# Kernel optimization log

Measured on AMD Instinct MI355X. Metric: run time of the kernel, lower is better.

Reference implementation:

```python
import jax, jax.numpy as jnp
import numpy as np

N, E, D = 20000, 320000, 256
BN_EPS = 1e-5


def _mlp(h, W1, b1, g, be, W2, b2, relu):
    # Linear(d, 2d) -> BatchNorm1d (training-mode batch stats) -> [ReLU] -> Linear(2d, d)
    h = h @ W1 + b1                              # [N, 2d]
    mu = h.mean(axis=0)
    var = h.var(axis=0)                          # biased, matches torch BN training normalization
    h = (h - mu) * jax.lax.rsqrt(var + BN_EPS) * g + be
    if relu:
        h = jax.nn.relu(h)
    return h @ W2 + b2                           # [N, d]


def _gine_conv(x, edge_index, edge_attr, W1, b1, g, be, W2, b2, relu):
    # PyG GINEConv with eps=0: nn((1+eps)*x + sum_j ReLU(x_j + e_ij))
    src, dst = edge_index[0], edge_index[1]
    msg = jax.nn.relu(x[src] + edge_attr)        # [E, d] gather + fuse
    agg = jax.ops.segment_sum(msg, dst, num_segments=x.shape[0])  # scatter-sum
    return _mlp(x + agg, W1, b1, g, be, W2, b2, relu)


def setup_inputs() -> dict:
    key = jax.random.key(0)
    ks = jax.random.split(key, 32)
    inp = {
        'x': jax.random.normal(ks[0], (N, D), dtype=jnp.float32),
        'edge_index': jax.random.randint(ks[1], (2, E), 0, N, dtype=jnp.int64),
        'edge_attr': jax.random.normal(ks[2], (E, D), dtype=jnp.float32),
        'noise': jax.random.normal(ks[3], (N, D), dtype=jnp.float32),
    }
    # 4 GINE convs: base_gcn, base_gcn2 (with ReLU), gcn_mean, gcn_logstddev (no ReLU)
    for i in range(4):
        k = 4 + 6 * i
        s1 = 1.0 / np.sqrt(D)
        s2 = 1.0 / np.sqrt(2 * D)
        inp[f'W1_{i}'] = jax.random.uniform(ks[k], (D, 2 * D), jnp.float32, -s1, s1)
        inp[f'b1_{i}'] = jax.random.uniform(ks[k + 1], (2 * D,), jnp.float32, -s1, s1)
        inp[f'g_{i}'] = jnp.ones((2 * D,), jnp.float32)
        inp[f'be_{i}'] = jnp.zeros((2 * D,), jnp.float32)
        inp[f'W2_{i}'] = jax.random.uniform(ks[k + 2], (2 * D, D), jnp.float32, -s2, s2)
        inp[f'b2_{i}'] = jax.random.uniform(ks[k + 3], (D,), jnp.float32, -s2, s2)
    return inp


def reference(x, edge_index, edge_attr, noise,
              W1_0, b1_0, g_0, be_0, W2_0, b2_0,
              W1_1, b1_1, g_1, be_1, W2_1, b2_1,
              W1_2, b1_2, g_2, be_2, W2_2, b2_2,
              W1_3, b1_3, g_3, be_3, W2_3, b2_3):
    h = _gine_conv(x, edge_index, edge_attr, W1_0, b1_0, g_0, be_0, W2_0, b2_0, True)
    h = _gine_conv(h, edge_index, edge_attr, W1_1, b1_1, g_1, be_1, W2_1, b2_1, True)
    mean = _gine_conv(h, edge_index, edge_attr, W1_2, b1_2, g_2, be_2, W2_2, b2_2, False)
    logstd = _gine_conv(h, edge_index, edge_attr, W1_3, b1_3, g_3, be_3, W2_3, b2_3, False)
    sampled_z = noise * jnp.exp(logstd) + mean   # reparameterization
    kl = 0.5 / sampled_z.shape[0] * (
        (1.0 + 2.0 * logstd - mean ** 2 - jnp.exp(logstd) ** 2).sum(axis=1).mean()
    )
    return sampled_z, mean, logstd, kl
```

## Files before the change

kernel.cpp:

```cpp
#include <hip/hip_runtime.h>

#define NNODES 20000
#define NEDGES 320000
#define DIM 256
#define DIM2 512
#define MPAD 20096
#define BN_EPS 1e-5f
#define NDTOT (NNODES * DIM)

typedef __attribute__((ext_vector_type(8))) short bf16x8;
typedef __attribute__((ext_vector_type(4))) float f32x4;

typedef __attribute__((address_space(1))) const unsigned char gconst_byte;
typedef __attribute__((address_space(3))) unsigned char lds_byte;

__device__ inline ushort f2bf(float f) {
    unsigned u = __float_as_uint(f);
    u += 0x7FFF + ((u >> 16) & 1);
    return (ushort)(u >> 16);
}
__device__ inline float bf2f(ushort u) {
    return __uint_as_float(((unsigned)u) << 16);
}

__global__ void hist_kernel(const int* __restrict__ ei, int* __restrict__ cnt) {
    int e = blockIdx.x * blockDim.x + threadIdx.x;
    if (e < NEDGES) atomicAdd(&cnt[ei[NEDGES + e]], 1);
}

__global__ __launch_bounds__(256) void scan_kernel(const int* __restrict__ cnt,
                                                   int* __restrict__ off,
                                                   int* __restrict__ cur,
                                                   float* __restrict__ klP) {
    int t = threadIdx.x;
    const int CH = (NNODES + 255) / 256;
    int b0 = t * CH, b1 = min(b0 + CH, NNODES);
    int s = 0;
    for (int i = b0; i < b1; ++i) s += cnt[i];
    __shared__ int sums[256];
    sums[t] = s;
    __syncthreads();
    if (t == 0) {
        int acc = 0;
        for (int i = 0; i < 256; ++i) { int tmp = sums[i]; sums[i] = acc; acc += tmp; }
        off[NNODES] = acc;
        klP[0] = 0.f;
    }
    __syncthreads();
    int run = sums[t];
    for (int i = b0; i < b1; ++i) {
        off[i] = run;
        cur[i] = run;
        run += cnt[i];
    }
}

__global__ void scatter_kernel(const int* __restrict__ ei, int* __restrict__ cur,
                               int* __restrict__ perm_e, int* __restrict__ perm_s) {
    int e = blockIdx.x * blockDim.x + threadIdx.x;
    if (e >= NEDGES) return;
    int d = ei[NEDGES + e];
    int pos = atomicAdd(&cur[d], 1);
    perm_e[pos] = e;
    perm_s[pos] = ei[e];
}

template<bool XF32, bool EAPERM, bool WEA>
__global__ __launch_bounds__(256) void agg_kernel(
        const float* __restrict__ Xf, const ushort* __restrict__ Xh,
        const float* __restrict__ EAf, const ushort* __restrict__ EAh,
        ushort* __restrict__ EAout,
        const int* __restrict__ off, const int* __restrict__ perm_e,
        const int* __restrict__ perm_s, ushort* __restrict__ A16) {
    int wid = (blockIdx.x * blockDim.x + threadIdx.x) >> 6;
    if (wid >= NNODES) return;
    int l = threadIdx.x & 63;
    int s0 = off[wid], s1 = off[wid + 1];
    float4 acc;
    if (XF32) {
        acc = *(const float4*)(Xf + (size_t)wid * DIM + l * 4);
    } else {
        ushort4 v = *(const ushort4*)(Xh + (size_t)wid * DIM + l * 4);
        acc = make_float4(bf2f(v.x), bf2f(v.y), bf2f(v.z), bf2f(v.w));
    }
    #pragma unroll 2
    for (int i = s0; i < s1; ++i) {
        int s = perm_s[i];
        float4 xr, er;
        if (XF32) {
            xr = *(const float4*)(Xf + (size_t)s * DIM + l * 4);
        } else {
            ushort4 v = *(const ushort4*)(Xh + (size_t)s * DIM + l * 4);
            xr = make_float4(bf2f(v.x), bf2f(v.y), bf2f(v.z), bf2f(v.w));
        }
        if (EAPERM) {
            ushort4 v = *(const ushort4*)(EAh + (size_t)i * DIM + l * 4);
            er = make_float4(bf2f(v.x), bf2f(v.y), bf2f(v.z), bf2f(v.w));
        } else {
            int e = perm_e[i];
            er = *(const float4*)(EAf + (size_t)e * DIM + l * 4);
        }
        if (WEA) {
            ushort4 o;
            o.x = f2bf(er.x); o.y = f2bf(er.y); o.z = f2bf(er.z); o.w = f2bf(er.w);
            *(ushort4*)(EAout + (size_t)i * DIM + l * 4) = o;
        }
        acc.x += fmaxf(xr.x + er.x, 0.f);
        acc.y += fmaxf(xr.y + er.y, 0.f);
        acc.z += fmaxf(xr.z + er.z, 0.f);
        acc.w += fmaxf(xr.w + er.w, 0.f);
    }
    ushort4 o;
    o.x = f2bf(acc.x); o.y = f2bf(acc.y); o.z = f2bf(acc.z); o.w = f2bf(acc.w);
    *(ushort4*)(A16 + (size_t)wid * DIM + l * 4) = o;
}

struct WPtrs {
    const float* w[8];
    ushort* o[8];
    int K[8];
    int Nc[8];
};
__global__ __launch_bounds__(256) void wconv_kernel(WPtrs p) {
    int w = blockIdx.x >> 9;
    int idx = ((blockIdx.x & 511) << 8) + threadIdx.x;
    int K = p.K[w], Nc = p.Nc[w];
    int oc = idx / K, ok = idx - oc * K;
    p.o[w][idx] = f2bf(p.w[w][(size_t)ok * Nc + oc]);
}

__global__ __launch_bounds__(64) void wfold_kernel(
        const ushort* __restrict__ WT2_2, const ushort* __restrict__ WT2_3,
        const float* __restrict__ stats,
        const float* __restrict__ g2, const float* __restrict__ be2,
        const float* __restrict__ g3, const float* __restrict__ be3,
        const float* __restrict__ b2_2, const float* __restrict__ b2_3,
        ushort* __restrict__ W2f, float* __restrict__ b2f) {
    const int l = blockIdx.x >> 8;
    const int n = blockIdx.x & 255;
    const int lane = threadIdx.x;
    const float invN = 1.0f / (float)NNODES;
    const ushort* WT = l ? WT2_3 : WT2_2;
    const float* gp = l ? g3 : g2;
    const float* bp = l ? be3 : be2;
    float part = 0.f;
    #pragma unroll
    for (int j = 0; j < 8; ++j) {
        int k = j * 64 + lane;
        int c = l * DIM2 + k;
        float mu = stats[c] * invN;
        float var = stats[1024 + c] * invN - mu * mu;
        float sc = gp[k] * rsqrtf(var + BN_EPS);
        float sh = bp[k] - mu * sc;
        float wv = bf2f(WT[(size_t)n * DIM2 + k]);
        W2f[(size_t)l * 131072 + (size_t)n * DIM2 + k] = f2bf(sc * wv);
        part += sh * wv;
    }
    #pragma unroll
    for (int o = 32; o > 0; o >>= 1) part += __shfl_down(part, o);
    if (lane == 0) b2f[l * 256 + n] = (l ? b2_3[n] : b2_2[n]) + part;
}

template<int K, bool OUT_BF16, bool STATS, bool FINAL>
__global__ __launch_bounds__(256) void mfma_gemm(
        const ushort* __restrict__ A16, int lda,
        const ushort* __restrict__ WT,
        const float* __restrict__ bias, const float* __restrict__ bias2,
        float* __restrict__ Cf, ushort* __restrict__ C16, int ldc,
        float* __restrict__ stats, int Nc, int Mlimit,
        const float* __restrict__ meanP, const float* __restrict__ noiseP,
        float* __restrict__ zP, float* __restrict__ klP) {
    __shared__ ushort As[128 * 64];
    __shared__ ushort Bs[128 * 64];
    const int tid = threadIdx.x;
    const int lane = tid & 63;
    const int wv = tid >> 6, wr = wv >> 1, wc = wv & 1;
    const int l15 = lane & 15, lhi = lane >> 4;
    const int r0 = blockIdx.y * 128, c0 = blockIdx.x * 128;

    const int srow = lane >> 3;
    const int scol = ((lane & 7) ^ srow) * 8;
    const int smask = (l15 & 7) << 4;

    f32x4 acc[4][4] = {};

    for (int k0 = 0; k0 < K; k0 += 64) {
        #pragma unroll
        for (int j = 0; j < 4; ++j) {
            const int jp = j * 4 + wv;
            const ushort* ga = A16 + (size_t)(r0 + jp * 8 + srow) * lda + k0 + scol;
            const ushort* gb = WT + (size_t)(c0 + jp * 8 + srow) * K + k0 + scol;
            __builtin_amdgcn_global_load_lds(
                (gconst_byte*)ga, (lds_byte*)((char*)As + jp * 1024), 16, 0, 0);
            __builtin_amdgcn_global_load_lds(
                (gconst_byte*)gb, (lds_byte*)((char*)Bs + jp * 1024), 16, 0, 0);
        }
        __syncthreads();
        #pragma unroll
        for (int kk = 0; kk < 2; ++kk) {
            bf16x8 a[4], b[4];
            #pragma unroll
            for (int m = 0; m < 4; ++m)
                a[m] = *(const bf16x8*)((const char*)As +
                        (wr * 64 + m * 16 + l15) * 128 + ((kk * 64 + lhi * 16) ^ smask));
            #pragma unroll
            for (int n = 0; n < 4; ++n)
                b[n] = *(const bf16x8*)((const char*)Bs +
                        (wc * 64 + n * 16 + l15) * 128 + ((kk * 64 + lhi * 16) ^ smask));
            #pragma unroll
            for (int m = 0; m < 4; ++m)
                #pragma unroll
                for (int n = 0; n < 4; ++n)
                    acc[m][n] = __builtin_amdgcn_mfma_f32_16x16x32_bf16(
                        a[m], b[n], acc[m][n], 0, 0, 0);
        }
        __syncthreads();
    }

    float bv[4];
    #pragma unroll
    for (int n = 0; n < 4; ++n) {
        int gc = c0 + wc * 64 + n * 16 + l15;
        bv[n] = (gc < DIM2) ? bias[gc] : bias2[gc - DIM2];
    }
    float sm[4] = {0.f, 0.f, 0.f, 0.f}, sq[4] = {0.f, 0.f, 0.f, 0.f};
    float kl = 0.f;
    #pragma unroll
    for (int m = 0; m < 4; ++m) {
        #pragma unroll
        for (int q = 0; q < 4; ++q) {
            int gr = r0 + wr * 64 + m * 16 + lhi * 4 + q;
            if (gr >= Mlimit) continue;
            #pragma unroll
            for (int n = 0; n < 4; ++n) {
                int gc = c0 + wc * 64 + n * 16 + l15;
                float v = acc[m][n][q] + bv[n];
                if (OUT_BF16) C16[(size_t)gr * ldc + gc] = f2bf(v);
                else          Cf[(size_t)gr * ldc + gc] = v;
                if (STATS) { sm[n] += v; sq[n] += v * v; }
                if (FINAL) {
                    size_t idx = (size_t)gr * DIM + gc;
                    float mean = meanP[idx];
                    float nz = noiseP[idx];
                    float e = expf(v);
                    zP[idx] = nz * e + mean;
                    kl += 1.f + 2.f * v - mean * mean - e * e;
                }
            }
        }
    }
    if (STATS) {
        #pragma unroll
        for (int n = 0; n < 4; ++n) {
            float sv = sm[n], qv = sq[n];
            sv += __shfl_xor(sv, 16); sv += __shfl_xor(sv, 32);
            qv += __shfl_xor(qv, 16); qv += __shfl_xor(qv, 32);
            if (lane < 16) {
                int gc = c0 + wc * 64 + n * 16 + l15;
                atomicAdd(&stats[gc], sv);
                atomicAdd(&stats[Nc + gc], qv);
            }
        }
    }
    if (FINAL) {
        #pragma unroll
        for (int o = 32; o > 0; o >>= 1) kl += __shfl_down(kl, o);
        if (lane == 0) {
            const float scale = 0.5f / ((float)NNODES * (float)NNODES);
            atomicAdd(klP, kl * scale);
        }
    }
}

template<int NCOLS>
__global__ __launch_bounds__(256) void bn_apply_kernel(
        ushort* __restrict__ H16, const float* __restrict__ stats,
        const float* __restrict__ g0, const float* __restrict__ be0) {
    const float invN = 1.0f / (float)NNODES;
    const int n4 = NNODES * NCOLS / 4;
    for (int i = blockIdx.x * blockDim.x + threadIdx.x; i < n4;
         i += gridDim.x * blockDim.x) {
        int cbase = (i * 4) & (NCOLS - 1);
        ushort4 u = ((const ushort4*)H16)[i];
        float vv[4] = {bf2f(u.x), bf2f(u.y), bf2f(u.z), bf2f(u.w)};
        #pragma unroll
        for (int k = 0; k < 4; ++k) {
            int c = cbase + k;
            float mu = stats[c] * invN;
            float var = stats[NCOLS + c] * invN - mu * mu;
            float x = (vv[k] - mu) * rsqrtf(var + BN_EPS) * g0[c] + be0[c];
            vv[k] = fmaxf(x, 0.f);
        }
        ushort4 o;
        o.x = f2bf(vv[0]); o.y = f2bf(vv[1]); o.z = f2bf(vv[2]); o.w = f2bf(vv[3]);
        ((ushort4*)H16)[i] = o;
    }
}

extern "C" void kernel_launch(void* const* d_in, const int* in_sizes, int n_in,
                              void* d_out, int out_size, void* d_ws, size_t ws_size,
                              hipStream_t stream) {
    const float* x     = (const float*)d_in[0];
    const int*   ei    = (const int*)d_in[1];
    const float* ea    = (const float*)d_in[2];
    const float* noise = (const float*)d_in[3];
    const float *W1[4], *b1[4], *g[4], *be[4], *W2[4], *b2[4];
    for (int i = 0; i < 4; ++i) {
        W1[i] = (const float*)d_in[4 + 6 * i];
        b1[i] = (const float*)d_in[5 + 6 * i];
        g[i]  = (const float*)d_in[6 + 6 * i];
        be[i] = (const float*)d_in[7 + 6 * i];
        W2[i] = (const float*)d_in[8 + 6 * i];
        b2[i] = (const float*)d_in[9 + 6 * i];
    }
    float* out = (float*)d_out;
    float* klP = out + 3 * NDTOT;

    char* p = (char*)d_ws;
    auto carve = [&](size_t bytes) {
        char* r = p;
        p += (bytes + 255) & ~(size_t)255;
        return r;
    };
    ushort* Braw16 = (ushort*)carve((size_t)MPAD * 1024 * 2);
    ushort* H16    = (ushort*)carve((size_t)MPAD * DIM * 2);
    ushort* A16    = (ushort*)carve((size_t)MPAD * DIM * 2);
    ushort* WT16   = (ushort*)carve((size_t)8 * 131072 * 2);
    ushort* W2f    = (ushort*)carve((size_t)2 * 131072 * 2);
    float*  b2f    = (float*)carve(512 * 4);
    float*  stats  = (float*)carve(4096 * 4 + NNODES * 4);
    int*    cnt    = (int*)(stats + 4096);
    int*    off    = (int*)carve((NNODES + 8) * 4);
    int*    cur    = (int*)carve(NNODES * 4);
    int*    perm_e = (int*)carve(NEDGES * 4);
    int*    perm_s = (int*)carve(NEDGES * 4);
    size_t baseBytes = (size_t)(p - (char*)d_ws);
    ushort* ea16 = (ushort*)p;
    const bool useEa16 = (baseBytes + (size_t)NEDGES * DIM * 2) <= ws_size;

    const int edgeGrid = (NEDGES + 255) / 256;
    const int aggGrid = (NNODES * 64) / 256;

    WPtrs wp;
    for (int i = 0; i < 4; ++i) {
        wp.w[i] = W1[i];     wp.o[i] = WT16 + (size_t)i * 131072;
        wp.K[i] = DIM;       wp.Nc[i] = DIM2;
        wp.w[4 + i] = W2[i]; wp.o[4 + i] = WT16 + (size_t)(4 + i) * 131072;
        wp.K[4 + i] = DIM2;  wp.Nc[4 + i] = DIM;
    }
    hipLaunchKernelGGL(wconv_kernel, dim3(8 * 512), dim3(256), 0, stream, wp);

    hipMemsetAsync(stats, 0, 4096 * 4 + NNODES * 4, stream);
    hipLaunchKernelGGL(hist_kernel, dim3(edgeGrid), dim3(256), 0, stream, ei, cnt);
    hipLaunchKernelGGL(scan_kernel, dim3(1), dim3(256), 0, stream, cnt, off, cur, klP);
    hipLaunchKernelGGL(scatter_kernel, dim3(edgeGrid), dim3(256), 0, stream,
                       ei, cur, perm_e, perm_s);

    dim3 blk(256);
    dim3 gemm1Grid(DIM2 / 128, MPAD / 128);
    dim3 gemm1WGrid(1024 / 128, MPAD / 128);
    dim3 gemm2Grid(DIM / 128, MPAD / 128);
    const float* nf = nullptr;
    float* nfm = nullptr;

    if (useEa16)
        hipLaunchKernelGGL((agg_kernel<true, false, true>), dim3(aggGrid), blk, 0, stream,
                           x, (const ushort*)nullptr, ea, (const ushort*)nullptr, ea16,
                           off, perm_e, perm_s, A16);
    else
        hipLaunchKernelGGL((agg_kernel<true, false, false>), dim3(aggGrid), blk, 0, stream,
                           x, (const ushort*)nullptr, ea, (const ushort*)nullptr, (ushort*)nullptr,
                           off, perm_e, perm_s, A16);
    hipLaunchKernelGGL((mfma_gemm<DIM, true, true, false>), gemm1Grid, blk, 0, stream,
                       A16, DIM, WT16, b1[0], b1[0],
                       nfm, Braw16, DIM2, stats, DIM2, NNODES, nf, nf, nfm, nfm);
    hipLaunchKernelGGL((bn_apply_kernel<DIM2>), dim3(2048), blk, 0, stream,
                       Braw16, stats, g[0], be[0]);
    hipLaunchKernelGGL((mfma_gemm<DIM2, true, false, false>), gemm2Grid, blk, 0, stream,
                       Braw16, DIM2, WT16 + 4 * 131072, b2[0], b2[0],
                       nfm, H16, DIM, nfm, DIM, NNODES, nf, nf, nfm, nfm);

    if (useEa16)
        hipLaunchKernelGGL((agg_kernel<false, true, false>), dim3(aggGrid), blk, 0, stream,
                           (const float*)nullptr, H16, (const float*)nullptr, ea16, (ushort*)nullptr,
                           off, perm_e, perm_s, A16);
    else
        hipLaunchKernelGGL((agg_kernel<false, false, false>), dim3(aggGrid), blk, 0, stream,
                           (const float*)nullptr, H16, ea, (const ushort*)nullptr, (ushort*)nullptr,
                           off, perm_e, perm_s, A16);
    hipLaunchKernelGGL((mfma_gemm<DIM, true, true, false>), gemm1Grid, blk, 0, stream,
                       A16, DIM, WT16 + 1 * 131072, b1[1], b1[1],
                       nfm, Braw16, DIM2, stats + 1024, DIM2, NNODES, nf, nf, nfm, nfm);
    hipLaunchKernelGGL((bn_apply_kernel<DIM2>), dim3(2048), blk, 0, stream,
                       Braw16, stats + 1024, g[1], be[1]);
    hipLaunchKernelGGL((mfma_gemm<DIM2, true, false, false>), gemm2Grid, blk, 0, stream,
                       Braw16, DIM2, WT16 + 5 * 131072, b2[1], b2[1],
                       nfm, H16, DIM, nfm, DIM, NNODES, nf, nf, nfm, nfm);

    if (useEa16)
        hipLaunchKernelGGL((agg_kernel<false, true, false>), dim3(aggGrid), blk, 0, stream,
                           (const float*)nullptr, H16, (const float*)nullptr, ea16, (ushort*)nullptr,
                           off, perm_e, perm_s, A16);
    else
        hipLaunchKernelGGL((agg_kernel<false, false, false>), dim3(aggGrid), blk, 0, stream,
                           (const float*)nullptr, H16, ea, (const ushort*)nullptr, (ushort*)nullptr,
                           off, perm_e, perm_s, A16);
    hipLaunchKernelGGL((mfma_gemm<DIM, true, true, false>), gemm1WGrid, blk, 0, stream,
                       A16, DIM, WT16 + 2 * 131072, b1[2], b1[3],
                       nfm, Braw16, 1024, stats + 2048, 1024, NNODES, nf, nf, nfm, nfm);
    hipLaunchKernelGGL(wfold_kernel, dim3(512), dim3(64), 0, stream,
                       WT16 + 6 * 131072, WT16 + 7 * 131072, stats + 2048,
                       g[2], be[2], g[3], be[3], b2[2], b2[3], W2f, b2f);
    hipLaunchKernelGGL((mfma_gemm<DIM2, false, false, false>), gemm2Grid, blk, 0, stream,
                       Braw16, 1024, W2f, b2f, b2f,
                       out + NDTOT, (ushort*)nullptr, DIM, nfm, DIM, NNODES, nf, nf, nfm, nfm);
    hipLaunchKernelGGL((mfma_gemm<DIM2, false, false, true>), gemm2Grid, blk, 0, stream,
                       Braw16 + 512, 1024, W2f + 131072, b2f + 256, b2f + 256,
                       out + 2 * NDTOT, (ushort*)nullptr, DIM, nfm, DIM, NNODES,
                       out + NDTOT, noise, out, klP);
}
```

Measured before the change: 517.1 us.

## Prefetch edge rows in aggregation, tile weight transpose, narrow GEMM2 column tiles

The aggregation loop now software-pipelines its loads, fetching the next edge's source row and edge attribute while it accumulates the current one. The weight conversion kernel now transposes through a padded 64x64 shared-memory tile, so both global reads and writes are coalesced instead of strided. The GEMM kernel gains a BCOLS template parameter, and the second GEMM of each MLP uses 64-column tiles, doubling its block count over 256 CUs. Narrower tiles give more parallelism but less B reuse per block.

```diff
diff --git a/kernel.cpp b/kernel.cpp
--- a/kernel.cpp
+++ b/kernel.cpp
@@ -76,30 +76,31 @@
     if (wid >= NNODES) return;
     int l = threadIdx.x & 63;
     int s0 = off[wid], s1 = off[wid + 1];
-    float4 acc;
-    if (XF32) {
-        acc = *(const float4*)(Xf + (size_t)wid * DIM + l * 4);
-    } else {
-        ushort4 v = *(const ushort4*)(Xh + (size_t)wid * DIM + l * 4);
-        acc = make_float4(bf2f(v.x), bf2f(v.y), bf2f(v.z), bf2f(v.w));
-    }
-    #pragma unroll 2
-    for (int i = s0; i < s1; ++i) {
-        int s = perm_s[i];
-        float4 xr, er;
-        if (XF32) {
-            xr = *(const float4*)(Xf + (size_t)s * DIM + l * 4);
-        } else {
-            ushort4 v = *(const ushort4*)(Xh + (size_t)s * DIM + l * 4);
-            xr = make_float4(bf2f(v.x), bf2f(v.y), bf2f(v.z), bf2f(v.w));
-        }
+
+    auto loadX = [&](int s) -> float4 {
+        if (XF32) return *(const float4*)(Xf + (size_t)s * DIM + l * 4);
+        ushort4 v = *(const ushort4*)(Xh + (size_t)s * DIM + l * 4);
+        return make_float4(bf2f(v.x), bf2f(v.y), bf2f(v.z), bf2f(v.w));
+    };
+    auto loadE = [&](int i) -> float4 {
         if (EAPERM) {
             ushort4 v = *(const ushort4*)(EAh + (size_t)i * DIM + l * 4);
-            er = make_float4(bf2f(v.x), bf2f(v.y), bf2f(v.z), bf2f(v.w));
-        } else {
-            int e = perm_e[i];
-            er = *(const float4*)(EAf + (size_t)e * DIM + l * 4);
-        }
+            return make_float4(bf2f(v.x), bf2f(v.y), bf2f(v.z), bf2f(v.w));
+        }
+        int e = perm_e[i];
+        return *(const float4*)(EAf + (size_t)e * DIM + l * 4);
+    };
+
+    float4 acc = loadX(wid);
+    if (!XF32) {  }
+
+    int i = s0;
+    float4 xc, ec;
+    if (i < s1) { xc = loadX(perm_s[i]); ec = loadE(i); }
+    while (i < s1) {
+        float4 xr = xc, er = ec;
+        int inext = i + 1;
+        if (inext < s1) { xc = loadX(perm_s[inext]); ec = loadE(inext); }
         if (WEA) {
             ushort4 o;
             o.x = f2bf(er.x); o.y = f2bf(er.y); o.z = f2bf(er.z); o.w = f2bf(er.w);
@@ -109,6 +110,7 @@
         acc.y += fmaxf(xr.y + er.y, 0.f);
         acc.z += fmaxf(xr.z + er.z, 0.f);
         acc.w += fmaxf(xr.w + er.w, 0.f);
+        i = inext;
     }
     ushort4 o;
     o.x = f2bf(acc.x); o.y = f2bf(acc.y); o.z = f2bf(acc.z); o.w = f2bf(acc.w);
@@ -122,11 +124,27 @@
     int Nc[8];
 };
 __global__ __launch_bounds__(256) void wconv_kernel(WPtrs p) {
-    int w = blockIdx.x >> 9;
-    int idx = ((blockIdx.x & 511) << 8) + threadIdx.x;
+    __shared__ float T[64][65];
+    int w = blockIdx.x >> 5;
+    int tile = blockIdx.x & 31;
     int K = p.K[w], Nc = p.Nc[w];
-    int oc = idx / K, ok = idx - oc * K;
-    p.o[w][idx] = f2bf(p.w[w][(size_t)ok * Nc + oc]);
+    int tilesPerRow = Nc >> 6;
+    int tk = (tile / tilesPerRow) << 6;
+    int tc = (tile % tilesPerRow) << 6;
+    int tx = threadIdx.x & 63, ty = threadIdx.x >> 6;
+    const float* in = p.w[w];
+    #pragma unroll
+    for (int r = 0; r < 16; ++r) {
+        int kk = ty + r * 4;
+        T[kk][tx] = in[(size_t)(tk + kk) * Nc + tc + tx];
+    }
+    __syncthreads();
+    ushort* outp = p.o[w];
+    #pragma unroll
+    for (int r = 0; r < 16; ++r) {
+        int cc = ty + r * 4;
+        outp[(size_t)(tc + cc) * K + tk + tx] = f2bf(T[tx][cc]);
+    }
 }
 
 __global__ __launch_bounds__(64) void wfold_kernel(
@@ -161,7 +179,7 @@
     if (lane == 0) b2f[l * 256 + n] = (l ? b2_3[n] : b2_2[n]) + part;
 }
 
-template<int K, bool OUT_BF16, bool STATS, bool FINAL>
+template<int K, int BCOLS, bool OUT_BF16, bool STATS, bool FINAL>
 __global__ __launch_bounds__(256) void mfma_gemm(
         const ushort* __restrict__ A16, int lda,
         const ushort* __restrict__ WT,
@@ -170,60 +188,67 @@
         float* __restrict__ stats, int Nc, int Mlimit,
         const float* __restrict__ meanP, const float* __restrict__ noiseP,
         float* __restrict__ zP, float* __restrict__ klP) {
+    constexpr int NREP = BCOLS / 32;
     __shared__ ushort As[128 * 64];
-    __shared__ ushort Bs[128 * 64];
+    __shared__ ushort Bs[BCOLS * 64];
     const int tid = threadIdx.x;
     const int lane = tid & 63;
     const int wv = tid >> 6, wr = wv >> 1, wc = wv & 1;
     const int l15 = lane & 15, lhi = lane >> 4;
-    const int r0 = blockIdx.y * 128, c0 = blockIdx.x * 128;
+    const int r0 = blockIdx.y * 128, c0 = blockIdx.x * BCOLS;
 
     const int srow = lane >> 3;
     const int scol = ((lane & 7) ^ srow) * 8;
     const int smask = (l15 & 7) << 4;
 
-    f32x4 acc[4][4] = {};
+    f32x4 acc[4][NREP] = {};
 
     for (int k0 = 0; k0 < K; k0 += 64) {
         #pragma unroll
         for (int j = 0; j < 4; ++j) {
             const int jp = j * 4 + wv;
             const ushort* ga = A16 + (size_t)(r0 + jp * 8 + srow) * lda + k0 + scol;
+            __builtin_amdgcn_global_load_lds(
+                (gconst_byte*)ga, (lds_byte*)((char*)As + jp * 1024), 16, 0, 0);
+        }
+        #pragma unroll
+        for (int j = 0; j < BCOLS / 32; ++j) {
+            const int jp = j * 4 + wv;
             const ushort* gb = WT + (size_t)(c0 + jp * 8 + srow) * K + k0 + scol;
             __builtin_amdgcn_global_load_lds(
-                (gconst_byte*)ga, (lds_byte*)((char*)As + jp * 1024), 16, 0, 0);
-            __builtin_amdgcn_global_load_lds(
                 (gconst_byte*)gb, (lds_byte*)((char*)Bs + jp * 1024), 16, 0, 0);
         }
         __syncthreads();
         #pragma unroll
         for (int kk = 0; kk < 2; ++kk) {
-            bf16x8 a[4], b[4];
+            bf16x8 a[4], b[NREP];
             #pragma unroll
             for (int m = 0; m < 4; ++m)
                 a[m] = *(const bf16x8*)((const char*)As +
                         (wr * 64 + m * 16 + l15) * 128 + ((kk * 64 + lhi * 16) ^ smask));
             #pragma unroll
-            for (int n = 0; n < 4; ++n)
+            for (int n = 0; n < NREP; ++n)
                 b[n] = *(const bf16x8*)((const char*)Bs +
-                        (wc * 64 + n * 16 + l15) * 128 + ((kk * 64 + lhi * 16) ^ smask));
+                        (wc * (BCOLS / 2) + n * 16 + l15) * 128 + ((kk * 64 + lhi * 16) ^ smask));
             #pragma unroll
             for (int m = 0; m < 4; ++m)
                 #pragma unroll
-                for (int n = 0; n < 4; ++n)
+                for (int n = 0; n < NREP; ++n)
                     acc[m][n] = __builtin_amdgcn_mfma_f32_16x16x32_bf16(
                         a[m], b[n], acc[m][n], 0, 0, 0);
         }
         __syncthreads();
     }
 
-    float bv[4];
-    #pragma unroll
-    for (int n = 0; n < 4; ++n) {
-        int gc = c0 + wc * 64 + n * 16 + l15;
+    float bv[NREP];
+    #pragma unroll
+    for (int n = 0; n < NREP; ++n) {
+        int gc = c0 + wc * (BCOLS / 2) + n * 16 + l15;
         bv[n] = (gc < DIM2) ? bias[gc] : bias2[gc - DIM2];
     }
-    float sm[4] = {0.f, 0.f, 0.f, 0.f}, sq[4] = {0.f, 0.f, 0.f, 0.f};
+    float sm[NREP], sq[NREP];
+    #pragma unroll
+    for (int n = 0; n < NREP; ++n) { sm[n] = 0.f; sq[n] = 0.f; }
     float kl = 0.f;
     #pragma unroll
     for (int m = 0; m < 4; ++m) {
@@ -232,8 +257,8 @@
             int gr = r0 + wr * 64 + m * 16 + lhi * 4 + q;
             if (gr >= Mlimit) continue;
             #pragma unroll
-            for (int n = 0; n < 4; ++n) {
-                int gc = c0 + wc * 64 + n * 16 + l15;
+            for (int n = 0; n < NREP; ++n) {
+                int gc = c0 + wc * (BCOLS / 2) + n * 16 + l15;
                 float v = acc[m][n][q] + bv[n];
                 if (OUT_BF16) C16[(size_t)gr * ldc + gc] = f2bf(v);
                 else          Cf[(size_t)gr * ldc + gc] = v;
@@ -251,12 +276,12 @@
     }
     if (STATS) {
         #pragma unroll
-        for (int n = 0; n < 4; ++n) {
+        for (int n = 0; n < NREP; ++n) {
             float sv = sm[n], qv = sq[n];
             sv += __shfl_xor(sv, 16); sv += __shfl_xor(sv, 32);
             qv += __shfl_xor(qv, 16); qv += __shfl_xor(qv, 32);
             if (lane < 16) {
-                int gc = c0 + wc * 64 + n * 16 + l15;
+                int gc = c0 + wc * (BCOLS / 2) + n * 16 + l15;
                 atomicAdd(&stats[gc], sv);
                 atomicAdd(&stats[Nc + gc], qv);
             }
@@ -348,7 +373,7 @@
         wp.w[4 + i] = W2[i]; wp.o[4 + i] = WT16 + (size_t)(4 + i) * 131072;
         wp.K[4 + i] = DIM2;  wp.Nc[4 + i] = DIM;
     }
-    hipLaunchKernelGGL(wconv_kernel, dim3(8 * 512), dim3(256), 0, stream, wp);
+    hipLaunchKernelGGL(wconv_kernel, dim3(8 * 32), dim3(256), 0, stream, wp);
 
     hipMemsetAsync(stats, 0, 4096 * 4 + NNODES * 4, stream);
     hipLaunchKernelGGL(hist_kernel, dim3(edgeGrid), dim3(256), 0, stream, ei, cnt);
@@ -359,7 +384,7 @@
     dim3 blk(256);
     dim3 gemm1Grid(DIM2 / 128, MPAD / 128);
     dim3 gemm1WGrid(1024 / 128, MPAD / 128);
-    dim3 gemm2Grid(DIM / 128, MPAD / 128);
+    dim3 gemm2Grid(DIM / 64, MPAD / 128);
     const float* nf = nullptr;
     float* nfm = nullptr;
 
@@ -371,12 +396,12 @@
         hipLaunchKernelGGL((agg_kernel<true, false, false>), dim3(aggGrid), blk, 0, stream,
                            x, (const ushort*)nullptr, ea, (const ushort*)nullptr, (ushort*)nullptr,
                            off, perm_e, perm_s, A16);
-    hipLaunchKernelGGL((mfma_gemm<DIM, true, true, false>), gemm1Grid, blk, 0, stream,
+    hipLaunchKernelGGL((mfma_gemm<DIM, 128, true, true, false>), gemm1Grid, blk, 0, stream,
                        A16, DIM, WT16, b1[0], b1[0],
                        nfm, Braw16, DIM2, stats, DIM2, NNODES, nf, nf, nfm, nfm);
     hipLaunchKernelGGL((bn_apply_kernel<DIM2>), dim3(2048), blk, 0, stream,
                        Braw16, stats, g[0], be[0]);
-    hipLaunchKernelGGL((mfma_gemm<DIM2, true, false, false>), gemm2Grid, blk, 0, stream,
+    hipLaunchKernelGGL((mfma_gemm<DIM2, 64, true, false, false>), gemm2Grid, blk, 0, stream,
                        Braw16, DIM2, WT16 + 4 * 131072, b2[0], b2[0],
                        nfm, H16, DIM, nfm, DIM, NNODES, nf, nf, nfm, nfm);
 
@@ -388,12 +413,12 @@
         hipLaunchKernelGGL((agg_kernel<false, false, false>), dim3(aggGrid), blk, 0, stream,
                            (const float*)nullptr, H16, ea, (const ushort*)nullptr, (ushort*)nullptr,
                            off, perm_e, perm_s, A16);
-    hipLaunchKernelGGL((mfma_gemm<DIM, true, true, false>), gemm1Grid, blk, 0, stream,
+    hipLaunchKernelGGL((mfma_gemm<DIM, 128, true, true, false>), gemm1Grid, blk, 0, stream,
                        A16, DIM, WT16 + 1 * 131072, b1[1], b1[1],
                        nfm, Braw16, DIM2, stats + 1024, DIM2, NNODES, nf, nf, nfm, nfm);
     hipLaunchKernelGGL((bn_apply_kernel<DIM2>), dim3(2048), blk, 0, stream,
                        Braw16, stats + 1024, g[1], be[1]);
-    hipLaunchKernelGGL((mfma_gemm<DIM2, true, false, false>), gemm2Grid, blk, 0, stream,
+    hipLaunchKernelGGL((mfma_gemm<DIM2, 64, true, false, false>), gemm2Grid, blk, 0, stream,
                        Braw16, DIM2, WT16 + 5 * 131072, b2[1], b2[1],
                        nfm, H16, DIM, nfm, DIM, NNODES, nf, nf, nfm, nfm);
 
@@ -405,16 +430,16 @@
         hipLaunchKernelGGL((agg_kernel<false, false, false>), dim3(aggGrid), blk, 0, stream,
                            (const float*)nullptr, H16, ea, (const ushort*)nullptr, (ushort*)nullptr,
                            off, perm_e, perm_s, A16);
-    hipLaunchKernelGGL((mfma_gemm<DIM, true, true, false>), gemm1WGrid, blk, 0, stream,
+    hipLaunchKernelGGL((mfma_gemm<DIM, 128, true, true, false>), gemm1WGrid, blk, 0, stream,
                        A16, DIM, WT16 + 2 * 131072, b1[2], b1[3],
                        nfm, Braw16, 1024, stats + 2048, 1024, NNODES, nf, nf, nfm, nfm);
     hipLaunchKernelGGL(wfold_kernel, dim3(512), dim3(64), 0, stream,
                        WT16 + 6 * 131072, WT16 + 7 * 131072, stats + 2048,
                        g[2], be[2], g[3], be[3], b2[2], b2[3], W2f, b2f);
-    hipLaunchKernelGGL((mfma_gemm<DIM2, false, false, false>), gemm2Grid, blk, 0, stream,
+    hipLaunchKernelGGL((mfma_gemm<DIM2, 64, false, false, false>), gemm2Grid, blk, 0, stream,
                        Braw16, 1024, W2f, b2f, b2f,
                        out + NDTOT, (ushort*)nullptr, DIM, nfm, DIM, NNODES, nf, nf, nfm, nfm);
-    hipLaunchKernelGGL((mfma_gemm<DIM2, false, false, true>), gemm2Grid, blk, 0, stream,
+    hipLaunchKernelGGL((mfma_gemm<DIM2, 64, false, false, true>), gemm2Grid, blk, 0, stream,
                        Braw16 + 512, 1024, W2f + 131072, b2f + 256, b2f + 256,
                        out + 2 * NDTOT, (ushort*)nullptr, DIM, nfm, DIM, NNODES,
                        out + NDTOT, noise, out, klP);
```

Result: slower. 553.5 us (+7.0%).
